# Kernel tuning notes

Hardware: AMD Instinct MI355X
Metric: run time of the kernel (lower is better)

The kernel has to match this reference:

```python
import jax, jax.numpy as jnp
import numpy as np

N_NODES = 200000
D = 128            # in_channels
B_GRAPHS = 512     # batch_size
STEPS = 3          # processing_steps


def setup_inputs() -> dict:
    key = jax.random.key(0)
    k = jax.random.split(key, 6)
    x = jax.random.normal(k[0], (N_NODES, D), dtype=jnp.float32)
    batch = jnp.sort(jax.random.randint(k[1], (N_NODES,), 0, B_GRAPHS, dtype=jnp.int64))
    s = 0.1
    W_ih = jax.random.normal(k[2], (3 * D, 2 * D), dtype=jnp.float32) * s
    W_hh = jax.random.normal(k[3], (3 * D, D), dtype=jnp.float32) * s
    b_ih = jax.random.normal(k[4], (3 * D,), dtype=jnp.float32) * s
    b_hh = jax.random.normal(k[5], (3 * D,), dtype=jnp.float32) * s
    return {"x": x, "batch": batch, "batch_size": B_GRAPHS,
            "W_ih": W_ih, "W_hh": W_hh, "b_ih": b_ih, "b_hh": b_hh}


def _gru_cell(inp, h, W_ih, W_hh, b_ih, b_hh):
    # inp: [B, 2d], h: [B, d]; PyTorch GRU gate order: r, z, n
    gi = inp @ W_ih.T + b_ih  # [B, 3d]
    gh = h @ W_hh.T + b_hh    # [B, 3d]
    gi_r, gi_z, gi_n = jnp.split(gi, 3, axis=-1)
    gh_r, gh_z, gh_n = jnp.split(gh, 3, axis=-1)
    r = jax.nn.sigmoid(gi_r + gh_r)
    z = jax.nn.sigmoid(gi_z + gh_z)
    n = jnp.tanh(gi_n + r * gh_n)
    return (1.0 - z) * n + z * h


def reference(x, batch, batch_size, W_ih, W_hh, b_ih, b_hh):
    B = batch_size
    d = x.shape[1]
    h = jnp.zeros((B, d), dtype=x.dtype)
    q_star = jnp.zeros((B, 2 * d), dtype=x.dtype)
    for _ in range(STEPS):
        h = _gru_cell(q_star, h, W_ih, W_hh, b_ih, b_hh)
        q = h  # num_layers=1: output == new hidden state
        e = jnp.sum(x * q[batch], axis=-1)  # [N]
        m = jax.ops.segment_max(e, batch, num_segments=B)
        ex = jnp.exp(e - m[batch])
        s = jax.ops.segment_sum(ex, batch, num_segments=B)
        a = ex / (s[batch] + 1e-16)  # segment softmax weights [N]
        r = jax.ops.segment_sum(a[:, None] * x, batch, num_segments=B)  # [B, d]
        q_star = jnp.concatenate([q, r], axis=-1)
    return q_star
```

## Files before the change

### kernel.cpp

```cpp
#include <hip/hip_runtime.h>
#include <math.h>
#include <float.h>

constexpr int D = 128;
constexpr int B = 512;
constexpr int STEPS = 3;
constexpr int NW_IH = 3 * D * 2 * D;
constexpr int NW_HH = 3 * D * D;
constexpr float NEG_HUGE = -3.402823466e38f;

__device__ __forceinline__ float sigmoidf_(float x) { return 1.f / (1.f + __expf(-x)); }
__device__ __forceinline__ float bflo(unsigned int u) { return __uint_as_float(u << 16); }
__device__ __forceinline__ float bfhi(unsigned int u) { return __uint_as_float(u & 0xffff0000u); }
__device__ __forceinline__ unsigned short f2bf_rn(float f) {
    unsigned int u = __float_as_uint(f);
    u += 0x7fffu + ((u >> 16) & 1u);
    return (unsigned short)(u >> 16);
}
__device__ __forceinline__ float4 ld4(const float* p) { return *(const float4*)p; }
__device__ __forceinline__ int imin_(int a, int b) { return a < b ? a : b; }

__global__ __launch_bounds__(256) void k_prep(const float* __restrict__ Wih,
        const float* __restrict__ Whh, const int* __restrict__ batch, int n,
        unsigned short* __restrict__ wih_bf, unsigned short* __restrict__ whh_bf,
        int* __restrict__ seg) {
    int i = blockIdx.x * blockDim.x + threadIdx.x;
    if (i < NW_IH) wih_bf[i] = f2bf_rn(Wih[i]);
    else if (i < NW_IH + NW_HH) whh_bf[i - NW_IH] = f2bf_rn(Whh[i - NW_IH]);
    if (i <= B) {
        int lo = 0, hi = n;
        while (lo < hi) { int mid = (lo + hi) >> 1; if (batch[mid] < i) lo = mid + 1; else hi = mid; }
        seg[i] = lo;
    }
}

struct Trip { float4 a0, a1, b0, b1, c0, c1, d0, d1; };

__global__ __launch_bounds__(256, 2) void k_set2set(
        const float* __restrict__ x,
        const unsigned short* __restrict__ wih_bf,
        const unsigned short* __restrict__ whh_bf,
        const float* __restrict__ bih, const float* __restrict__ bhh,
        const int* __restrict__ seg, float* __restrict__ out) {
    __shared__ __align__(16) float s_q[2 * D];
    __shared__ __align__(16) float s_h[D];
    __shared__ float s_gi[3 * D], s_gh[3 * D];
    __shared__ float sm[16], sl[16];
    __shared__ __align__(16) float rpart[4][D];

    const int b = blockIdx.x;
    const int tid = threadIdx.x;
    const int start = seg[b], end = seg[b + 1];
    const int g = tid >> 4;
    const int s = tid & 15;
    const int s4 = s * 4;

    const int len = end - start;
    const int FT = (len + 63) >> 6;
    const int gbase = start + g;
    const int eclamp = (len > 0) ? end - 1 : start;

    float m_run, l_run;
    float4 acc0, acc1;
    float4 q0, q1;
    Trip T0_, T1_;

    auto load_trip = [&](Trip& T, int t) {
        const int n0 = gbase + (t << 6);
        const float* p0 = x + ((size_t)imin_(n0,      eclamp) << 7) + s4;
        const float* p1 = x + ((size_t)imin_(n0 + 16, eclamp) << 7) + s4;
        const float* p2 = x + ((size_t)imin_(n0 + 32, eclamp) << 7) + s4;
        const float* p3 = x + ((size_t)imin_(n0 + 48, eclamp) << 7) + s4;
        T.a0 = ld4(p0); T.a1 = ld4(p0 + 64);
        T.b0 = ld4(p1); T.b1 = ld4(p1 + 64);
        T.c0 = ld4(p2); T.c1 = ld4(p2 + 64);
        T.d0 = ld4(p3); T.d1 = ld4(p3 + 64);
    };
    auto dot8 = [&](const float4& lo, const float4& hi) {
        float p = lo.x * q0.x;
        p = fmaf(lo.y, q0.y, p); p = fmaf(lo.z, q0.z, p); p = fmaf(lo.w, q0.w, p);
        p = fmaf(hi.x, q1.x, p); p = fmaf(hi.y, q1.y, p);
        p = fmaf(hi.z, q1.z, p); p = fmaf(hi.w, q1.w, p);
        return p;
    };
    auto compute_core = [&](const Trip& T, bool masked, int t) {
        float p0 = dot8(T.a0, T.a1);
        float p1 = dot8(T.b0, T.b1);
        float p2 = dot8(T.c0, T.c1);
        float p3 = dot8(T.d0, T.d1);
        p0 += __shfl_xor(p0, 1, 64); p1 += __shfl_xor(p1, 1, 64);
        p2 += __shfl_xor(p2, 1, 64); p3 += __shfl_xor(p3, 1, 64);
        p0 += __shfl_xor(p0, 2, 64); p1 += __shfl_xor(p1, 2, 64);
        p2 += __shfl_xor(p2, 2, 64); p3 += __shfl_xor(p3, 2, 64);
        p0 += __shfl_xor(p0, 4, 64); p1 += __shfl_xor(p1, 4, 64);
        p2 += __shfl_xor(p2, 4, 64); p3 += __shfl_xor(p3, 4, 64);
        p0 += __shfl_xor(p0, 8, 64); p1 += __shfl_xor(p1, 8, 64);
        p2 += __shfl_xor(p2, 8, 64); p3 += __shfl_xor(p3, 8, 64);
        bool m0 = true, m1 = true, m2 = true, m3 = true;
        float h0 = p0, h1 = p1, h2 = p2, h3 = p3;
        if (masked) {
            const int n0 = gbase + (t << 6);
            m0 = n0 < end; m1 = n0 + 16 < end; m2 = n0 + 32 < end; m3 = n0 + 48 < end;
            h0 = m0 ? p0 : NEG_HUGE; h1 = m1 ? p1 : NEG_HUGE;
            h2 = m2 ? p2 : NEG_HUGE; h3 = m3 ? p3 : NEG_HUGE;
        }
        float nm = fmaxf(m_run, fmaxf(fmaxf(h0, h1), fmaxf(h2, h3)));
        float sc = __expf(m_run - nm);
        float e0 = __expf(p0 - nm), e1 = __expf(p1 - nm);
        float e2 = __expf(p2 - nm), e3 = __expf(p3 - nm);
        if (masked) {
            e0 = m0 ? e0 : 0.f; e1 = m1 ? e1 : 0.f;
            e2 = m2 ? e2 : 0.f; e3 = m3 ? e3 : 0.f;
        }
        l_run = fmaf(l_run, sc, (e0 + e1) + (e2 + e3));
        acc0.x = fmaf(acc0.x, sc, fmaf(e0, T.a0.x, fmaf(e1, T.b0.x, fmaf(e2, T.c0.x, e3 * T.d0.x))));
        acc0.y = fmaf(acc0.y, sc, fmaf(e0, T.a0.y, fmaf(e1, T.b0.y, fmaf(e2, T.c0.y, e3 * T.d0.y))));
        acc0.z = fmaf(acc0.z, sc, fmaf(e0, T.a0.z, fmaf(e1, T.b0.z, fmaf(e2, T.c0.z, e3 * T.d0.z))));
        acc0.w = fmaf(acc0.w, sc, fmaf(e0, T.a0.w, fmaf(e1, T.b0.w, fmaf(e2, T.c0.w, e3 * T.d0.w))));
        acc1.x = fmaf(acc1.x, sc, fmaf(e0, T.a1.x, fmaf(e1, T.b1.x, fmaf(e2, T.c1.x, e3 * T.d1.x))));
        acc1.y = fmaf(acc1.y, sc, fmaf(e0, T.a1.y, fmaf(e1, T.b1.y, fmaf(e2, T.c1.y, e3 * T.d1.y))));
        acc1.z = fmaf(acc1.z, sc, fmaf(e0, T.a1.z, fmaf(e1, T.b1.z, fmaf(e2, T.c1.z, e3 * T.d1.z))));
        acc1.w = fmaf(acc1.w, sc, fmaf(e0, T.a1.w, fmaf(e1, T.b1.w, fmaf(e2, T.c1.w, e3 * T.d1.w))));
        m_run = nm;
    };
    auto compute  = [&](const Trip& T)        { compute_core(T, false, 0); };
    auto computeM = [&](const Trip& T, int t) { compute_core(T, true,  t); };

    if (tid < 2 * D) s_q[tid] = 0.f;
    if (tid < D) s_h[tid] = 0.f;
    __syncthreads();

    for (int step = 0; step < STEPS; ++step) {
        if (FT > 0) load_trip(T0_, 0);

        if (step == 0) {
            for (int i = tid; i < 3 * D; i += 256) { s_gi[i] = bih[i]; s_gh[i] = bhh[i]; }
        } else if (tid < 192) {
            const int r0 = tid * 2, r1 = r0 + 1;
            float gi0 = bih[r0], gi1 = bih[r1];
            float gh0 = bhh[r0], gh1 = bhh[r1];
            const float4* q4 = (const float4*)s_q;
            const float4* h4 = (const float4*)s_h;
            const uint4* w0 = (const uint4*)(wih_bf + (size_t)r0 * (2 * D));
            const uint4* w1 = (const uint4*)(wih_bf + (size_t)r1 * (2 * D));
#pragma unroll 4
            for (int c = 0; c < 32; ++c) {
                uint4 wa = w0[c], wb = w1[c];
                float4 qa = q4[2 * c], qb = q4[2 * c + 1];
                gi0 = fmaf(bflo(wa.x), qa.x, gi0); gi0 = fmaf(bfhi(wa.x), qa.y, gi0);
                gi0 = fmaf(bflo(wa.y), qa.z, gi0); gi0 = fmaf(bfhi(wa.y), qa.w, gi0);
                gi0 = fmaf(bflo(wa.z), qb.x, gi0); gi0 = fmaf(bfhi(wa.z), qb.y, gi0);
                gi0 = fmaf(bflo(wa.w), qb.z, gi0); gi0 = fmaf(bfhi(wa.w), qb.w, gi0);
                gi1 = fmaf(bflo(wb.x), qa.x, gi1); gi1 = fmaf(bfhi(wb.x), qa.y, gi1);
                gi1 = fmaf(bflo(wb.y), qa.z, gi1); gi1 = fmaf(bfhi(wb.y), qa.w, gi1);
                gi1 = fmaf(bflo(wb.z), qb.x, gi1); gi1 = fmaf(bfhi(wb.z), qb.y, gi1);
                gi1 = fmaf(bflo(wb.w), qb.z, gi1); gi1 = fmaf(bfhi(wb.w), qb.w, gi1);
            }
            const uint4* v0 = (const uint4*)(whh_bf + (size_t)r0 * D);
            const uint4* v1 = (const uint4*)(whh_bf + (size_t)r1 * D);
#pragma unroll 4
            for (int c = 0; c < 16; ++c) {
                uint4 wa = v0[c], wb = v1[c];
                float4 ha = h4[2 * c], hb = h4[2 * c + 1];
                gh0 = fmaf(bflo(wa.x), ha.x, gh0); gh0 = fmaf(bfhi(wa.x), ha.y, gh0);
                gh0 = fmaf(bflo(wa.y), ha.z, gh0); gh0 = fmaf(bfhi(wa.y), ha.w, gh0);
                gh0 = fmaf(bflo(wa.z), hb.x, gh0); gh0 = fmaf(bfhi(wa.z), hb.y, gh0);
                gh0 = fmaf(bflo(wa.w), hb.z, gh0); gh0 = fmaf(bfhi(wa.w), hb.w, gh0);
                gh1 = fmaf(bflo(wb.x), ha.x, gh1); gh1 = fmaf(bfhi(wb.x), ha.y, gh1);
                gh1 = fmaf(bflo(wb.y), ha.z, gh1); gh1 = fmaf(bfhi(wb.y), ha.w, gh1);
                gh1 = fmaf(bflo(wb.z), hb.x, gh1); gh1 = fmaf(bfhi(wb.z), hb.y, gh1);
                gh1 = fmaf(bflo(wb.w), hb.z, gh1); gh1 = fmaf(bfhi(wb.w), hb.w, gh1);
            }
            s_gi[r0] = gi0; s_gi[r1] = gi1;
            s_gh[r0] = gh0; s_gh[r1] = gh1;
        }
        __syncthreads();
        if (tid < D) {
            const int t = tid;
            float r  = sigmoidf_(s_gi[t] + s_gh[t]);
            float z  = sigmoidf_(s_gi[D + t] + s_gh[D + t]);
            float nn = tanhf(s_gi[2 * D + t] + r * s_gh[2 * D + t]);
            float hn = (1.f - z) * nn + z * s_h[t];
            s_h[t] = hn;
            s_q[t] = hn;
        }
        __syncthreads();

        q0 = ((const float4*)s_h)[s];
        q1 = ((const float4*)s_h)[16 + s];
        m_run = NEG_HUGE; l_run = 0.f;
        acc0 = make_float4(0.f, 0.f, 0.f, 0.f);
        acc1 = make_float4(0.f, 0.f, 0.f, 0.f);

        if (FT > 0) {
            if (FT > 1) load_trip(T1_, 1);
            int t = 0;
            for (; t + 2 < FT; t += 2) {
                compute(T0_); load_trip(T0_, t + 2);
                compute(T1_); if (t + 3 < FT) load_trip(T1_, t + 3);
            }
            if (t == FT - 1) computeM(T0_, t);
            else { compute(T0_); computeM(T1_, t + 1); }
        }

        if (s == 0) { sm[g] = m_run; sl[g] = l_run; }
        __syncthreads();

        {
            const float mv = sm[s];
            const float lv = sl[s];
            float M = mv;
            M = fmaxf(M, __shfl_xor(M, 1, 64));
            M = fmaxf(M, __shfl_xor(M, 2, 64));
            M = fmaxf(M, __shfl_xor(M, 4, 64));
            M = fmaxf(M, __shfl_xor(M, 8, 64));
            float term = lv * __expf(mv - M);
            term += __shfl_xor(term, 1, 64);
            term += __shfl_xor(term, 2, 64);
            term += __shfl_xor(term, 4, 64);
            term += __shfl_xor(term, 8, 64);
            const float inv = 1.f / (term + 1e-16f);
            const float fac = __expf(m_run - M) * inv;
            acc0.x *= fac; acc0.y *= fac; acc0.z *= fac; acc0.w *= fac;
            acc1.x *= fac; acc1.y *= fac; acc1.z *= fac; acc1.w *= fac;
        }
        acc0.x += __shfl_xor(acc0.x, 16, 64); acc0.y += __shfl_xor(acc0.y, 16, 64);
        acc0.z += __shfl_xor(acc0.z, 16, 64); acc0.w += __shfl_xor(acc0.w, 16, 64);
        acc1.x += __shfl_xor(acc1.x, 16, 64); acc1.y += __shfl_xor(acc1.y, 16, 64);
        acc1.z += __shfl_xor(acc1.z, 16, 64); acc1.w += __shfl_xor(acc1.w, 16, 64);
        acc0.x += __shfl_xor(acc0.x, 32, 64); acc0.y += __shfl_xor(acc0.y, 32, 64);
        acc0.z += __shfl_xor(acc0.z, 32, 64); acc0.w += __shfl_xor(acc0.w, 32, 64);
        acc1.x += __shfl_xor(acc1.x, 32, 64); acc1.y += __shfl_xor(acc1.y, 32, 64);
        acc1.z += __shfl_xor(acc1.z, 32, 64); acc1.w += __shfl_xor(acc1.w, 32, 64);

        const int wv = tid >> 6;
        if ((tid & 63) < 16) {
            *(float4*)&rpart[wv][s4]      = acc0;
            *(float4*)&rpart[wv][64 + s4] = acc1;
        }
        __syncthreads();
        if (tid < D) {
            float v = (rpart[0][tid] + rpart[1][tid]) + (rpart[2][tid] + rpart[3][tid]);
            s_q[D + tid] = v;
        }
        __syncthreads();
    }

    if (tid < 2 * D) out[(size_t)b * (2 * D) + tid] = s_q[tid];
}

extern "C" void kernel_launch(void* const* d_in, const int* in_sizes, int n_in,
                              void* d_out, int out_size, void* d_ws, size_t ws_size,
                              hipStream_t stream) {
    const float* x    = (const float*)d_in[0];
    const int*   batch= (const int*)d_in[1];
    const float* Wih  = (const float*)d_in[3];
    const float* Whh  = (const float*)d_in[4];
    const float* bih  = (const float*)d_in[5];
    const float* bhh  = (const float*)d_in[6];
    const int n = in_sizes[0] / D;

    char* ws = (char*)d_ws;
    int* seg = (int*)ws;
    unsigned short* wih_bf = (unsigned short*)(ws + 4096);
    unsigned short* whh_bf = (unsigned short*)(ws + 4096 + (size_t)NW_IH * 2);

    const int total = NW_IH + NW_HH;
    k_prep<<<(total + 255) / 256, 256, 0, stream>>>(Wih, Whh, batch, n, wih_bf, whh_bf, seg);
    k_set2set<<<B, 256, 0, stream>>>(x, wih_bf, whh_bf, bih, bhh, seg, (float*)d_out);
}
```

Measured before the change: 220.0 us.

## Cache fp16 copy of x during first step and reuse it in later steps

During the first attention step, each block writes a half-precision copy of its node features to workspace while it reads the fp32 input. Steps two and three read this fp16 copy instead of the fp32 x, which halves their memory traffic. In exchange, step 0 does extra global writes and the attention math in later steps runs on rounded inputs, which adds numerical error and needs a larger workspace.

```diff
diff --git a/kernel.cpp b/kernel.cpp
--- a/kernel.cpp
+++ b/kernel.cpp
@@ -1,4 +1,5 @@
 #include <hip/hip_runtime.h>
+#include <hip/hip_fp16.h>
 #include <math.h>
 #include <float.h>
 
@@ -19,6 +20,17 @@
 }
 __device__ __forceinline__ float4 ld4(const float* p) { return *(const float4*)p; }
 __device__ __forceinline__ int imin_(int a, int b) { return a < b ? a : b; }
+
+__device__ __forceinline__ unsigned int packh2(float a, float b) {
+    union { __half2 h; unsigned int u; } c;
+    c.h = __floats2half2_rn(a, b);
+    return c.u;
+}
+__device__ __forceinline__ float2 unpackh2(unsigned int u) {
+    union { unsigned int u; __half2 h; } c;
+    c.u = u;
+    return __half22float2(c.h);
+}
 
 __global__ __launch_bounds__(256) void k_prep(const float* __restrict__ Wih,
         const float* __restrict__ Whh, const int* __restrict__ batch, int n,
@@ -41,7 +53,8 @@
         const unsigned short* __restrict__ wih_bf,
         const unsigned short* __restrict__ whh_bf,
         const float* __restrict__ bih, const float* __restrict__ bhh,
-        const int* __restrict__ seg, float* __restrict__ out) {
+        const int* __restrict__ seg, unsigned short* __restrict__ xh,
+        float* __restrict__ out) {
     __shared__ __align__(16) float s_q[2 * D];
     __shared__ __align__(16) float s_h[D];
     __shared__ float s_gi[3 * D], s_gh[3 * D];
@@ -54,6 +67,7 @@
     const int g = tid >> 4;
     const int s = tid & 15;
     const int s4 = s * 4;
+    const int s8 = s * 8;
 
     const int len = end - start;
     const int FT = (len + 63) >> 6;
@@ -65,7 +79,7 @@
     float4 q0, q1;
     Trip T0_, T1_;
 
-    auto load_trip = [&](Trip& T, int t) {
+    auto load_trip32 = [&](Trip& T, int t) {
         const int n0 = gbase + (t << 6);
         const float* p0 = x + ((size_t)imin_(n0,      eclamp) << 7) + s4;
         const float* p1 = x + ((size_t)imin_(n0 + 16, eclamp) << 7) + s4;
@@ -75,6 +89,46 @@
         T.b0 = ld4(p1); T.b1 = ld4(p1 + 64);
         T.c0 = ld4(p2); T.c1 = ld4(p2 + 64);
         T.d0 = ld4(p3); T.d1 = ld4(p3 + 64);
+    };
+    auto store_trip16 = [&](const Trip& T, int t) {
+        const int n0 = gbase + (t << 6);
+        uint4 v;
+        v.x = packh2(T.a0.x, T.a0.y); v.y = packh2(T.a0.z, T.a0.w);
+        v.z = packh2(T.a1.x, T.a1.y); v.w = packh2(T.a1.z, T.a1.w);
+        *(uint4*)(xh + ((size_t)imin_(n0, eclamp) << 7) + s8) = v;
+        v.x = packh2(T.b0.x, T.b0.y); v.y = packh2(T.b0.z, T.b0.w);
+        v.z = packh2(T.b1.x, T.b1.y); v.w = packh2(T.b1.z, T.b1.w);
+        *(uint4*)(xh + ((size_t)imin_(n0 + 16, eclamp) << 7) + s8) = v;
+        v.x = packh2(T.c0.x, T.c0.y); v.y = packh2(T.c0.z, T.c0.w);
+        v.z = packh2(T.c1.x, T.c1.y); v.w = packh2(T.c1.z, T.c1.w);
+        *(uint4*)(xh + ((size_t)imin_(n0 + 32, eclamp) << 7) + s8) = v;
+        v.x = packh2(T.d0.x, T.d0.y); v.y = packh2(T.d0.z, T.d0.w);
+        v.z = packh2(T.d1.x, T.d1.y); v.w = packh2(T.d1.z, T.d1.w);
+        *(uint4*)(xh + ((size_t)imin_(n0 + 48, eclamp) << 7) + s8) = v;
+    };
+    auto load_trip16 = [&](Trip& T, int t) {
+        const int n0 = gbase + (t << 6);
+        const uint4 va = *(const uint4*)(xh + ((size_t)imin_(n0,      eclamp) << 7) + s8);
+        const uint4 vb = *(const uint4*)(xh + ((size_t)imin_(n0 + 16, eclamp) << 7) + s8);
+        const uint4 vc = *(const uint4*)(xh + ((size_t)imin_(n0 + 32, eclamp) << 7) + s8);
+        const uint4 vd = *(const uint4*)(xh + ((size_t)imin_(n0 + 48, eclamp) << 7) + s8);
+        float2 f;
+        f = unpackh2(va.x); T.a0.x = f.x; T.a0.y = f.y;
+        f = unpackh2(va.y); T.a0.z = f.x; T.a0.w = f.y;
+        f = unpackh2(va.z); T.a1.x = f.x; T.a1.y = f.y;
+        f = unpackh2(va.w); T.a1.z = f.x; T.a1.w = f.y;
+        f = unpackh2(vb.x); T.b0.x = f.x; T.b0.y = f.y;
+        f = unpackh2(vb.y); T.b0.z = f.x; T.b0.w = f.y;
+        f = unpackh2(vb.z); T.b1.x = f.x; T.b1.y = f.y;
+        f = unpackh2(vb.w); T.b1.z = f.x; T.b1.w = f.y;
+        f = unpackh2(vc.x); T.c0.x = f.x; T.c0.y = f.y;
+        f = unpackh2(vc.y); T.c0.z = f.x; T.c0.w = f.y;
+        f = unpackh2(vc.z); T.c1.x = f.x; T.c1.y = f.y;
+        f = unpackh2(vc.w); T.c1.z = f.x; T.c1.w = f.y;
+        f = unpackh2(vd.x); T.d0.x = f.x; T.d0.y = f.y;
+        f = unpackh2(vd.y); T.d0.z = f.x; T.d0.w = f.y;
+        f = unpackh2(vd.z); T.d1.x = f.x; T.d1.y = f.y;
+        f = unpackh2(vd.w); T.d1.z = f.x; T.d1.w = f.y;
     };
     auto dot8 = [&](const float4& lo, const float4& hi) {
         float p = lo.x * q0.x;
@@ -131,7 +185,7 @@
     __syncthreads();
 
     for (int step = 0; step < STEPS; ++step) {
-        if (FT > 0) load_trip(T0_, 0);
+        if (FT > 0) { if (step == 0) load_trip32(T0_, 0); else load_trip16(T0_, 0); }
 
         if (step == 0) {
             for (int i = tid; i < 3 * D; i += 256) { s_gi[i] = bih[i]; s_gh[i] = bhh[i]; }
@@ -193,14 +247,29 @@
         acc1 = make_float4(0.f, 0.f, 0.f, 0.f);
 
         if (FT > 0) {
-            if (FT > 1) load_trip(T1_, 1);
-            int t = 0;
-            for (; t + 2 < FT; t += 2) {
-                compute(T0_); load_trip(T0_, t + 2);
-                compute(T1_); if (t + 3 < FT) load_trip(T1_, t + 3);
+            if (step == 0) {
+                if (FT > 1) load_trip32(T1_, 1);
+                int t = 0;
+                for (; t + 2 < FT; t += 2) {
+                    compute(T0_); store_trip16(T0_, t); load_trip32(T0_, t + 2);
+                    compute(T1_); store_trip16(T1_, t + 1);
+                    if (t + 3 < FT) load_trip32(T1_, t + 3);
+                }
+                if (t == FT - 1) { computeM(T0_, t); store_trip16(T0_, t); }
+                else {
+                    compute(T0_); store_trip16(T0_, t);
+                    computeM(T1_, t + 1); store_trip16(T1_, t + 1);
+                }
+            } else {
+                if (FT > 1) load_trip16(T1_, 1);
+                int t = 0;
+                for (; t + 2 < FT; t += 2) {
+                    compute(T0_); load_trip16(T0_, t + 2);
+                    compute(T1_); if (t + 3 < FT) load_trip16(T1_, t + 3);
+                }
+                if (t == FT - 1) computeM(T0_, t);
+                else { compute(T0_); computeM(T1_, t + 1); }
             }
-            if (t == FT - 1) computeM(T0_, t);
-            else { compute(T0_); computeM(T1_, t + 1); }
         }
 
         if (s == 0) { sm[g] = m_run; sl[g] = l_run; }
@@ -264,8 +333,9 @@
     int* seg = (int*)ws;
     unsigned short* wih_bf = (unsigned short*)(ws + 4096);
     unsigned short* whh_bf = (unsigned short*)(ws + 4096 + (size_t)NW_IH * 2);
+    unsigned short* xh     = (unsigned short*)(ws + 4096 + (size_t)NW_IH * 2 + (size_t)NW_HH * 2);
 
     const int total = NW_IH + NW_HH;
     k_prep<<<(total + 255) / 256, 256, 0, stream>>>(Wih, Whh, batch, n, wih_bf, whh_bf, seg);
-    k_set2set<<<B, 256, 0, stream>>>(x, wih_bf, whh_bf, bih, bhh, seg, (float*)d_out);
-}
+    k_set2set<<<B, 256, 0, stream>>>(x, wih_bf, whh_bf, bih, bhh, seg, xh, (float*)d_out);
+}
```

Result: slower. 238.9 us (+8.6%).

## Double block size to 512 threads and give each GRU gate row its own thread

Applied to the files above, without the earlier changes.

Raises the set2set block from 256 to 512 threads, so 32 groups of 16 lanes stream node rows with a stride of 128 per tile. The cross-group softmax merge and the r partial reduction are widened to cover 8 wavefronts. The GRU gate matvec now uses 384 threads with one row each instead of 192 threads with two rows, which shortens the serial dot-product chain. The aim is more memory-level parallelism per graph and a shorter GRU phase, at the cost of higher register pressure under the (512,4) launch bound and more idle threads in the serial sections.

```diff
diff --git a/kernel.cpp b/kernel.cpp
--- a/kernel.cpp
+++ b/kernel.cpp
@@ -36,7 +36,7 @@
 
 struct Trip { float4 a0, a1, b0, b1, c0, c1, d0, d1; };
 
-__global__ __launch_bounds__(256, 2) void k_set2set(
+__global__ __launch_bounds__(512, 4) void k_set2set(
         const float* __restrict__ x,
         const unsigned short* __restrict__ wih_bf,
         const unsigned short* __restrict__ whh_bf,
@@ -45,8 +45,8 @@
     __shared__ __align__(16) float s_q[2 * D];
     __shared__ __align__(16) float s_h[D];
     __shared__ float s_gi[3 * D], s_gh[3 * D];
-    __shared__ float sm[16], sl[16];
-    __shared__ __align__(16) float rpart[4][D];
+    __shared__ float sm[32], sl[32];
+    __shared__ __align__(16) float rpart[8][D];
 
     const int b = blockIdx.x;
     const int tid = threadIdx.x;
@@ -56,7 +56,7 @@
     const int s4 = s * 4;
 
     const int len = end - start;
-    const int FT = (len + 63) >> 6;
+    const int FT = (len + 127) >> 7;
     const int gbase = start + g;
     const int eclamp = (len > 0) ? end - 1 : start;
 
@@ -66,11 +66,11 @@
     Trip T0_, T1_;
 
     auto load_trip = [&](Trip& T, int t) {
-        const int n0 = gbase + (t << 6);
+        const int n0 = gbase + (t << 7);
         const float* p0 = x + ((size_t)imin_(n0,      eclamp) << 7) + s4;
-        const float* p1 = x + ((size_t)imin_(n0 + 16, eclamp) << 7) + s4;
-        const float* p2 = x + ((size_t)imin_(n0 + 32, eclamp) << 7) + s4;
-        const float* p3 = x + ((size_t)imin_(n0 + 48, eclamp) << 7) + s4;
+        const float* p1 = x + ((size_t)imin_(n0 + 32, eclamp) << 7) + s4;
+        const float* p2 = x + ((size_t)imin_(n0 + 64, eclamp) << 7) + s4;
+        const float* p3 = x + ((size_t)imin_(n0 + 96, eclamp) << 7) + s4;
         T.a0 = ld4(p0); T.a1 = ld4(p0 + 64);
         T.b0 = ld4(p1); T.b1 = ld4(p1 + 64);
         T.c0 = ld4(p2); T.c1 = ld4(p2 + 64);
@@ -99,8 +99,8 @@
         bool m0 = true, m1 = true, m2 = true, m3 = true;
         float h0 = p0, h1 = p1, h2 = p2, h3 = p3;
         if (masked) {
-            const int n0 = gbase + (t << 6);
-            m0 = n0 < end; m1 = n0 + 16 < end; m2 = n0 + 32 < end; m3 = n0 + 48 < end;
+            const int n0 = gbase + (t << 7);
+            m0 = n0 < end; m1 = n0 + 32 < end; m2 = n0 + 64 < end; m3 = n0 + 96 < end;
             h0 = m0 ? p0 : NEG_HUGE; h1 = m1 ? p1 : NEG_HUGE;
             h2 = m2 ? p2 : NEG_HUGE; h3 = m3 ? p3 : NEG_HUGE;
         }
@@ -134,45 +134,36 @@
         if (FT > 0) load_trip(T0_, 0);
 
         if (step == 0) {
-            for (int i = tid; i < 3 * D; i += 256) { s_gi[i] = bih[i]; s_gh[i] = bhh[i]; }
-        } else if (tid < 192) {
-            const int r0 = tid * 2, r1 = r0 + 1;
-            float gi0 = bih[r0], gi1 = bih[r1];
-            float gh0 = bhh[r0], gh1 = bhh[r1];
+            if (tid < 3 * D) { s_gi[tid] = bih[tid]; s_gh[tid] = bhh[tid]; }
+        } else if (tid < 384) {
+            const int r = tid;
+            float gi = bih[r], gh = bhh[r];
+            const uint4* w = (const uint4*)(wih_bf + (size_t)r * (2 * D));
+            const uint4* v = (const uint4*)(whh_bf + (size_t)r * D);
             const float4* q4 = (const float4*)s_q;
             const float4* h4 = (const float4*)s_h;
-            const uint4* w0 = (const uint4*)(wih_bf + (size_t)r0 * (2 * D));
-            const uint4* w1 = (const uint4*)(wih_bf + (size_t)r1 * (2 * D));
-#pragma unroll 4
-            for (int c = 0; c < 32; ++c) {
-                uint4 wa = w0[c], wb = w1[c];
-                float4 qa = q4[2 * c], qb = q4[2 * c + 1];
-                gi0 = fmaf(bflo(wa.x), qa.x, gi0); gi0 = fmaf(bfhi(wa.x), qa.y, gi0);
-                gi0 = fmaf(bflo(wa.y), qa.z, gi0); gi0 = fmaf(bfhi(wa.y), qa.w, gi0);
-                gi0 = fmaf(bflo(wa.z), qb.x, gi0); gi0 = fmaf(bfhi(wa.z), qb.y, gi0);
-                gi0 = fmaf(bflo(wa.w), qb.z, gi0); gi0 = fmaf(bfhi(wa.w), qb.w, gi0);
-                gi1 = fmaf(bflo(wb.x), qa.x, gi1); gi1 = fmaf(bfhi(wb.x), qa.y, gi1);
-                gi1 = fmaf(bflo(wb.y), qa.z, gi1); gi1 = fmaf(bfhi(wb.y), qa.w, gi1);
-                gi1 = fmaf(bflo(wb.z), qb.x, gi1); gi1 = fmaf(bfhi(wb.z), qb.y, gi1);
-                gi1 = fmaf(bflo(wb.w), qb.z, gi1); gi1 = fmaf(bfhi(wb.w), qb.w, gi1);
-            }
-            const uint4* v0 = (const uint4*)(whh_bf + (size_t)r0 * D);
-            const uint4* v1 = (const uint4*)(whh_bf + (size_t)r1 * D);
 #pragma unroll 4
             for (int c = 0; c < 16; ++c) {
-                uint4 wa = v0[c], wb = v1[c];
+                uint4 wa = w[c];
+                uint4 wb = w[c + 16];
+                uint4 va = v[c];
+                float4 qa = q4[2 * c], qb = q4[2 * c + 1];
+                float4 qc = q4[32 + 2 * c], qd = q4[33 + 2 * c];
                 float4 ha = h4[2 * c], hb = h4[2 * c + 1];
-                gh0 = fmaf(bflo(wa.x), ha.x, gh0); gh0 = fmaf(bfhi(wa.x), ha.y, gh0);
-                gh0 = fmaf(bflo(wa.y), ha.z, gh0); gh0 = fmaf(bfhi(wa.y), ha.w, gh0);
-                gh0 = fmaf(bflo(wa.z), hb.x, gh0); gh0 = fmaf(bfhi(wa.z), hb.y, gh0);
-                gh0 = fmaf(bflo(wa.w), hb.z, gh0); gh0 = fmaf(bfhi(wa.w), hb.w, gh0);
-                gh1 = fmaf(bflo(wb.x), ha.x, gh1); gh1 = fmaf(bfhi(wb.x), ha.y, gh1);
-                gh1 = fmaf(bflo(wb.y), ha.z, gh1); gh1 = fmaf(bfhi(wb.y), ha.w, gh1);
-                gh1 = fmaf(bflo(wb.z), hb.x, gh1); gh1 = fmaf(bfhi(wb.z), hb.y, gh1);
-                gh1 = fmaf(bflo(wb.w), hb.z, gh1); gh1 = fmaf(bfhi(wb.w), hb.w, gh1);
+                gi = fmaf(bflo(wa.x), qa.x, gi); gi = fmaf(bfhi(wa.x), qa.y, gi);
+                gi = fmaf(bflo(wa.y), qa.z, gi); gi = fmaf(bfhi(wa.y), qa.w, gi);
+                gi = fmaf(bflo(wa.z), qb.x, gi); gi = fmaf(bfhi(wa.z), qb.y, gi);
+                gi = fmaf(bflo(wa.w), qb.z, gi); gi = fmaf(bfhi(wa.w), qb.w, gi);
+                gi = fmaf(bflo(wb.x), qc.x, gi); gi = fmaf(bfhi(wb.x), qc.y, gi);
+                gi = fmaf(bflo(wb.y), qc.z, gi); gi = fmaf(bfhi(wb.y), qc.w, gi);
+                gi = fmaf(bflo(wb.z), qd.x, gi); gi = fmaf(bfhi(wb.z), qd.y, gi);
+                gi = fmaf(bflo(wb.w), qd.z, gi); gi = fmaf(bfhi(wb.w), qd.w, gi);
+                gh = fmaf(bflo(va.x), ha.x, gh); gh = fmaf(bfhi(va.x), ha.y, gh);
+                gh = fmaf(bflo(va.y), ha.z, gh); gh = fmaf(bfhi(va.y), ha.w, gh);
+                gh = fmaf(bflo(va.z), hb.x, gh); gh = fmaf(bfhi(va.z), hb.y, gh);
+                gh = fmaf(bflo(va.w), hb.z, gh); gh = fmaf(bfhi(va.w), hb.w, gh);
             }
-            s_gi[r0] = gi0; s_gi[r1] = gi1;
-            s_gh[r0] = gh0; s_gh[r1] = gh1;
+            s_gi[r] = gi; s_gh[r] = gh;
         }
         __syncthreads();
         if (tid < D) {
@@ -207,18 +198,21 @@
         __syncthreads();
 
         {
-            const float mv = sm[s];
-            const float lv = sl[s];
+            const int l32i = tid & 31;
+            const float mv = sm[l32i];
+            const float lv = sl[l32i];
             float M = mv;
             M = fmaxf(M, __shfl_xor(M, 1, 64));
             M = fmaxf(M, __shfl_xor(M, 2, 64));
             M = fmaxf(M, __shfl_xor(M, 4, 64));
             M = fmaxf(M, __shfl_xor(M, 8, 64));
+            M = fmaxf(M, __shfl_xor(M, 16, 64));
             float term = lv * __expf(mv - M);
             term += __shfl_xor(term, 1, 64);
             term += __shfl_xor(term, 2, 64);
             term += __shfl_xor(term, 4, 64);
             term += __shfl_xor(term, 8, 64);
+            term += __shfl_xor(term, 16, 64);
             const float inv = 1.f / (term + 1e-16f);
             const float fac = __expf(m_run - M) * inv;
             acc0.x *= fac; acc0.y *= fac; acc0.z *= fac; acc0.w *= fac;
@@ -240,7 +234,8 @@
         }
         __syncthreads();
         if (tid < D) {
-            float v = (rpart[0][tid] + rpart[1][tid]) + (rpart[2][tid] + rpart[3][tid]);
+            float v = ((rpart[0][tid] + rpart[1][tid]) + (rpart[2][tid] + rpart[3][tid]))
+                    + ((rpart[4][tid] + rpart[5][tid]) + (rpart[6][tid] + rpart[7][tid]));
             s_q[D + tid] = v;
         }
         __syncthreads();
@@ -267,5 +262,5 @@
 
     const int total = NW_IH + NW_HH;
     k_prep<<<(total + 255) / 256, 256, 0, stream>>>(Wih, Whh, batch, n, wih_bf, whh_bf, seg);
-    k_set2set<<<B, 256, 0, stream>>>(x, wih_bf, whh_bf, bih, bhh, seg, (float*)d_out);
-}
+    k_set2set<<<B, 512, 0, stream>>>(x, wih_bf, whh_bf, bih, bhh, seg, (float*)d_out);
+}
```

Measured after the change: 343.5 us. +56.1%, slower.

## Stage node features into LDS via async global_load_lds double buffering

Applied to the files above, without the earlier changes.

Replaces the register-held double-buffered float4 loads of x with direct global-to-LDS asynchronous copies into two per-wave LDS buffers. Tiles are read back with inline ds_read_b128, and manual vmcnt waits keep one tile in flight while the current one is computed. Prefetching also starts before the GRU update of each step. The goal is to cut VGPR pressure and overlap memory latency with compute better in this bandwidth-heavy streaming loop. The cost is 64 KB of extra LDS per block and reliance on hand-placed waitcnts; the first read in each step has no explicit wait and depends on waits the compiler emits elsewhere.

```diff
diff --git a/kernel.cpp b/kernel.cpp
--- a/kernel.cpp
+++ b/kernel.cpp
@@ -8,6 +8,11 @@
 constexpr int NW_IH = 3 * D * 2 * D;
 constexpr int NW_HH = 3 * D * D;
 constexpr float NEG_HUGE = -3.402823466e38f;
+
+typedef float f32x4 __attribute__((ext_vector_type(4)));
+typedef __attribute__((address_space(1))) unsigned int gu32;
+typedef __attribute__((address_space(3))) unsigned int lu32;
+typedef __attribute__((address_space(3))) const unsigned char lchar;
 
 __device__ __forceinline__ float sigmoidf_(float x) { return 1.f / (1.f + __expf(-x)); }
 __device__ __forceinline__ float bflo(unsigned int u) { return __uint_as_float(u << 16); }
@@ -17,8 +22,16 @@
     u += 0x7fffu + ((u >> 16) & 1u);
     return (unsigned short)(u >> 16);
 }
-__device__ __forceinline__ float4 ld4(const float* p) { return *(const float4*)p; }
 __device__ __forceinline__ int imin_(int a, int b) { return a < b ? a : b; }
+
+__device__ __forceinline__ void gll16(const float* g, float* l) {
+    __builtin_amdgcn_global_load_lds((const gu32*)g, (lu32*)l, 16, 0, 0);
+}
+__device__ __forceinline__ unsigned lds_lo(const void* p) {
+    return (unsigned)(unsigned long long)(lchar*)p;
+}
+#define WAITVM8() asm volatile("s_waitcnt vmcnt(8)" ::: "memory")
+#define WAITVM0() asm volatile("s_waitcnt vmcnt(0)" ::: "memory")
 
 __global__ __launch_bounds__(256) void k_prep(const float* __restrict__ Wih,
         const float* __restrict__ Whh, const int* __restrict__ batch, int n,
@@ -34,7 +47,26 @@
     }
 }
 
-struct Trip { float4 a0, a1, b0, b1, c0, c1, d0, d1; };
+struct TripV { f32x4 a0, a1, b0, b1, c0, c1, d0, d1; };
+
+__device__ __forceinline__ TripV lds_read_trip(unsigned la) {
+    TripV T;
+    asm volatile(
+        "ds_read_b128 %0, %8 offset:0\n\t"
+        "ds_read_b128 %1, %8 offset:1024\n\t"
+        "ds_read_b128 %2, %8 offset:2048\n\t"
+        "ds_read_b128 %3, %8 offset:3072\n\t"
+        "ds_read_b128 %4, %8 offset:4096\n\t"
+        "ds_read_b128 %5, %8 offset:5120\n\t"
+        "ds_read_b128 %6, %8 offset:6144\n\t"
+        "ds_read_b128 %7, %8 offset:7168\n\t"
+        "s_waitcnt lgkmcnt(0)"
+        : "=&v"(T.a0), "=&v"(T.a1), "=&v"(T.b0), "=&v"(T.b1),
+          "=&v"(T.c0), "=&v"(T.c1), "=&v"(T.d0), "=&v"(T.d1)
+        : "v"(la));
+    __builtin_amdgcn_sched_barrier(0);
+    return T;
+}
 
 __global__ __launch_bounds__(256, 2) void k_set2set(
         const float* __restrict__ x,
@@ -47,6 +79,8 @@
     __shared__ float s_gi[3 * D], s_gh[3 * D];
     __shared__ float sm[16], sl[16];
     __shared__ __align__(16) float rpart[4][D];
+    __shared__ __align__(16) float s_bufA[4][2048];
+    __shared__ __align__(16) float s_bufB[4][2048];
 
     const int b = blockIdx.x;
     const int tid = threadIdx.x;
@@ -54,36 +88,46 @@
     const int g = tid >> 4;
     const int s = tid & 15;
     const int s4 = s * 4;
+    const int wv = tid >> 6;
+    const int lane = tid & 63;
 
     const int len = end - start;
     const int FT = (len + 63) >> 6;
     const int gbase = start + g;
     const int eclamp = (len > 0) ? end - 1 : start;
 
+    float* bufA = &s_bufA[wv][0];
+    float* bufB = &s_bufB[wv][0];
+    const unsigned laA = lds_lo(bufA) + lane * 16;
+    const unsigned laB = lds_lo(bufB) + lane * 16;
+
     float m_run, l_run;
     float4 acc0, acc1;
     float4 q0, q1;
-    Trip T0_, T1_;
-
-    auto load_trip = [&](Trip& T, int t) {
+
+    auto stage_trip = [&](float* buf, int t) {
         const int n0 = gbase + (t << 6);
         const float* p0 = x + ((size_t)imin_(n0,      eclamp) << 7) + s4;
         const float* p1 = x + ((size_t)imin_(n0 + 16, eclamp) << 7) + s4;
         const float* p2 = x + ((size_t)imin_(n0 + 32, eclamp) << 7) + s4;
         const float* p3 = x + ((size_t)imin_(n0 + 48, eclamp) << 7) + s4;
-        T.a0 = ld4(p0); T.a1 = ld4(p0 + 64);
-        T.b0 = ld4(p1); T.b1 = ld4(p1 + 64);
-        T.c0 = ld4(p2); T.c1 = ld4(p2 + 64);
-        T.d0 = ld4(p3); T.d1 = ld4(p3 + 64);
+        gll16(p0,      buf);
+        gll16(p0 + 64, buf + 256);
+        gll16(p1,      buf + 512);
+        gll16(p1 + 64, buf + 768);
+        gll16(p2,      buf + 1024);
+        gll16(p2 + 64, buf + 1280);
+        gll16(p3,      buf + 1536);
+        gll16(p3 + 64, buf + 1792);
     };
-    auto dot8 = [&](const float4& lo, const float4& hi) {
+    auto dot8 = [&](const f32x4& lo, const f32x4& hi) {
         float p = lo.x * q0.x;
         p = fmaf(lo.y, q0.y, p); p = fmaf(lo.z, q0.z, p); p = fmaf(lo.w, q0.w, p);
         p = fmaf(hi.x, q1.x, p); p = fmaf(hi.y, q1.y, p);
         p = fmaf(hi.z, q1.z, p); p = fmaf(hi.w, q1.w, p);
         return p;
     };
-    auto compute_core = [&](const Trip& T, bool masked, int t) {
+    auto compute_core = [&](const TripV& T, bool masked, int t) {
         float p0 = dot8(T.a0, T.a1);
         float p1 = dot8(T.b0, T.b1);
         float p2 = dot8(T.c0, T.c1);
@@ -123,15 +167,16 @@
         acc1.w = fmaf(acc1.w, sc, fmaf(e0, T.a1.w, fmaf(e1, T.b1.w, fmaf(e2, T.c1.w, e3 * T.d1.w))));
         m_run = nm;
     };
-    auto compute  = [&](const Trip& T)        { compute_core(T, false, 0); };
-    auto computeM = [&](const Trip& T, int t) { compute_core(T, true,  t); };
+    auto compute  = [&](const TripV& T)        { compute_core(T, false, 0); };
+    auto computeM = [&](const TripV& T, int t) { compute_core(T, true,  t); };
 
     if (tid < 2 * D) s_q[tid] = 0.f;
     if (tid < D) s_h[tid] = 0.f;
     __syncthreads();
 
     for (int step = 0; step < STEPS; ++step) {
-        if (FT > 0) load_trip(T0_, 0);
+        if (FT > 0) stage_trip(bufA, 0);
+        if (FT > 1) stage_trip(bufB, 1);
 
         if (step == 0) {
             for (int i = tid; i < 3 * D; i += 256) { s_gi[i] = bih[i]; s_gh[i] = bhh[i]; }
@@ -193,14 +238,27 @@
         acc1 = make_float4(0.f, 0.f, 0.f, 0.f);
 
         if (FT > 0) {
-            if (FT > 1) load_trip(T1_, 1);
             int t = 0;
-            for (; t + 2 < FT; t += 2) {
-                compute(T0_); load_trip(T0_, t + 2);
-                compute(T1_); if (t + 3 < FT) load_trip(T1_, t + 3);
+            while (true) {
+                {
+                    TripV T = lds_read_trip(laA);
+                    const bool st = (t + 2 < FT);
+                    if (st) stage_trip(bufA, t + 2);
+                    if (t == FT - 1) { computeM(T, t); break; }
+                    compute(T);
+                    if (st) { WAITVM8(); } else { WAITVM0(); }
+                    ++t;
+                }
+                {
+                    TripV T = lds_read_trip(laB);
+                    const bool st = (t + 2 < FT);
+                    if (st) stage_trip(bufB, t + 2);
+                    if (t == FT - 1) { computeM(T, t); break; }
+                    compute(T);
+                    if (st) { WAITVM8(); } else { WAITVM0(); }
+                    ++t;
+                }
             }
-            if (t == FT - 1) computeM(T0_, t);
-            else { compute(T0_); computeM(T1_, t + 1); }
         }
 
         if (s == 0) { sm[g] = m_run; sl[g] = l_run; }
@@ -233,7 +291,6 @@
         acc1.x += __shfl_xor(acc1.x, 32, 64); acc1.y += __shfl_xor(acc1.y, 32, 64);
         acc1.z += __shfl_xor(acc1.z, 32, 64); acc1.w += __shfl_xor(acc1.w, 32, 64);
 
-        const int wv = tid >> 6;
         if ((tid & 63) < 16) {
             *(float4*)&rpart[wv][s4]      = acc0;
             *(float4*)&rpart[wv][64 + s4] = acc1;
```

New measurement: 218.3 us. About the same (-0.8%).
